# Kernel optimization log

Measured on AMD Instinct MI355X. Metric: run time of the kernel, lower is better.

Reference implementation:

```python
import jax, jax.numpy as jnp
import numpy as np

NUM_HEADS = 8  # from init_kwargs
SR = 2         # sr_ratio from init_kwargs


def layernorm(t, g, b, eps=1e-5):
    mu = jnp.mean(t, axis=-1, keepdims=True)
    var = jnp.mean((t - mu) ** 2, axis=-1, keepdims=True)
    return (t - mu) * jax.lax.rsqrt(var + eps) * g + b


def setup_inputs() -> dict:
    key = jax.random.key(0)
    ks = jax.random.split(key, 6)
    B, C = 4, 256
    Hx = Wx = 64
    Hz = Wz = 32
    N = Hz * Wz + Hx * Wx  # 5120 (template tokens first, then search tokens)
    s = 0.02
    return {
        "x": jax.random.normal(ks[0], (B, N, C), jnp.float32),
        "Wq": jax.random.normal(ks[1], (C, C), jnp.float32) * s,          # nn.Linear(dim, dim, bias=False)
        "Wkv": jax.random.normal(ks[2], (2 * C, C), jnp.float32) * s,     # nn.Linear(dim, 2*dim, bias=False)
        "Wsr": jax.random.normal(ks[3], (C, C, SR, SR), jnp.float32) * s, # Conv2d(dim, dim, k=sr, stride=sr) OIHW
        "bsr": jnp.zeros((C,), jnp.float32),
        "gamma": jnp.ones((C,), jnp.float32),
        "beta": jnp.zeros((C,), jnp.float32),
        "Wproj": jax.random.normal(ks[4], (C, C), jnp.float32) * s,
        "bproj": jnp.zeros((C,), jnp.float32),
        "H_x": Hx, "W_x": Wx, "H_z": Hz, "W_z": Wz,
    }


def reference(x, Wq, Wkv, Wsr, bsr, gamma, beta, Wproj, bproj, H_x, W_x, H_z, W_z):
    B, N, C = x.shape
    h = NUM_HEADS
    d = C // h
    scale = d ** -0.5
    Nz, Nx = H_z * W_z, H_x * W_x

    # q for all tokens: [B, h, N, d]
    q = (x @ Wq.T).reshape(B, N, h, d).transpose(0, 2, 1, 3)

    # spatial reduction (sr_ratio > 1 branch): strided conv + layernorm on each stream
    z_tok, x_tok = x[:, :Nz], x[:, Nz:]
    ker = jnp.transpose(Wsr, (2, 3, 1, 0))  # OIHW -> HWIO

    def sr_branch(t, H, W):
        img = t.reshape(B, H, W, C)  # NHWC; same layout as torch NCHW reshape
        out = jax.lax.conv_general_dilated(
            img, ker, window_strides=(SR, SR), padding="VALID",
            dimension_numbers=("NHWC", "HWIO", "NHWC")) + bsr
        out = out.reshape(B, -1, C)
        return layernorm(out, gamma, beta)

    x_ = sr_branch(x_tok, H_x, W_x)  # [B, (Hx/sr)*(Wx/sr), C]
    z_ = sr_branch(z_tok, H_z, W_z)  # [B, (Hz/sr)*(Wz/sr), C]
    zL = z_.shape[1]
    cat = jnp.concatenate([z_, x_], axis=1)  # [B, L, C]

    kv = (cat @ Wkv.T).reshape(B, -1, 2, h, d).transpose(2, 0, 3, 1, 4)  # [2, B, h, L, d]
    k, v = kv[0], kv[1]

    q_z, q_x = q[:, :, :Nz], q[:, :, Nz:]
    k_z, v_z = k[:, :, :zL], v[:, :, :zL]

    # template queries attend only to reduced template keys/values
    attn_z = jax.nn.softmax(jnp.einsum("bhqd,bhkd->bhqk", q_z, k_z) * scale, axis=-1)
    out_z = jnp.einsum("bhqk,bhkd->bhqd", attn_z, v_z).transpose(0, 2, 1, 3).reshape(B, Nz, C)

    # search queries attend to full (template+search) reduced keys/values
    attn_x = jax.nn.softmax(jnp.einsum("bhqd,bhkd->bhqk", q_x, k) * scale, axis=-1)
    out_x = jnp.einsum("bhqk,bhkd->bhqd", attn_x, v).transpose(0, 2, 1, 3).reshape(B, Nx, C)

    out = jnp.concatenate([out_z, out_x], axis=1)
    return out @ Wproj.T + bproj
```

## Files before the change

### kernel.cpp

```cpp
#include <hip/hip_runtime.h>
#include <hip/hip_bf16.h>
#include <cstddef>

#define BATCH 4
#define CCH 256
#define NHEAD 8
#define DHEAD 32
#define NZ 1024
#define NX 4096
#define NTOK 5120
#define LKV 1280
#define QC 0.25503486f

typedef __attribute__((ext_vector_type(8))) short bf16x8;
typedef __attribute__((ext_vector_type(4))) float floatx4;

__device__ inline short f2bf(float f) {
  __hip_bfloat16 h = __float2bfloat16(f);
  return __builtin_bit_cast(short, h);
}
__device__ inline unsigned int pk2(float a, float b) {
  unsigned int lo = (unsigned short)f2bf(a);
  unsigned int hi = (unsigned short)f2bf(b);
  return lo | (hi << 16);
}
__device__ inline unsigned int pk2f(float a, float b) {
  unsigned int ua = __builtin_bit_cast(unsigned int, a) + 0x8000u;
  unsigned int ub = __builtin_bit_cast(unsigned int, b) + 0x8000u;
  return __builtin_amdgcn_perm(ub, ua, 0x07060302u);
}
__device__ inline void cvt8(const float* __restrict__ src, short* __restrict__ dst, int i) {
  float4 v0 = ((const float4*)src)[i * 2];
  float4 v1 = ((const float4*)src)[i * 2 + 1];
  uint4 u;
  u.x = pk2(v0.x, v0.y); u.y = pk2(v0.z, v0.w);
  u.z = pk2(v1.x, v1.y); u.w = pk2(v1.z, v1.w);
  ((uint4*)dst)[i] = u;
}

__global__ __launch_bounds__(256) void prep_weights(const float* __restrict__ Wq,
                                                    const float* __restrict__ Wkv,
                                                    const float* __restrict__ Wproj,
                                                    const float* __restrict__ Wsr,
                                                    const float* __restrict__ x,
                                                    short* __restrict__ Wqb,
                                                    short* __restrict__ Wkvb,
                                                    short* __restrict__ Wprojb,
                                                    short* __restrict__ Wkb,
                                                    short* __restrict__ xb) {
  int blk = blockIdx.x, tid = threadIdx.x;
  if (blk < 32) {
    cvt8(Wq, Wqb, blk * 256 + tid);
  } else if (blk < 96) {
    cvt8(Wkv, Wkvb, (blk - 32) * 256 + tid);
  } else if (blk < 128) {
    cvt8(Wproj, Wprojb, (blk - 96) * 256 + tid);
  } else if (blk < 1152) {
    int i = (blk - 128) * 256 + tid;
    int co = i >> 10;
    int rem = i & 1023;
    int di = rem >> 9, dj = (rem >> 8) & 1, ci = rem & 255;
    Wkb[i] = f2bf(Wsr[((co * 256 + ci) * 2 + di) * 2 + dj]);
  } else {
    cvt8(x, xb, (blk - 1152) * 256 + tid);
  }
}

#define G64_DECL()                                                           \
  __shared__ short As[64][72];                                               \
  __shared__ short Bs[64][72];                                               \
  int tid = threadIdx.x;                                                     \
  int wave = tid >> 6, lg = (tid & 63) >> 4, lr = tid & 15;                  \
  int sr = tid >> 2, sc = tid & 3;                                           \
  floatx4 acc[4] = {{0.f,0.f,0.f,0.f},{0.f,0.f,0.f,0.f},                     \
                    {0.f,0.f,0.f,0.f},{0.f,0.f,0.f,0.f}};

#define G64_MFMA8()                                                          \
    __syncthreads();                                                         \
    {                                                                        \
      bf16x8 af0 = *(bf16x8*)&As[wave * 16 + lr][lg * 8];                    \
      bf16x8 af1 = *(bf16x8*)&As[wave * 16 + lr][32 + lg * 8];               \
      _Pragma("unroll") for (int n = 0; n < 4; ++n) {                        \
        bf16x8 bf0 = *(bf16x8*)&Bs[n * 16 + lr][lg * 8];                     \
        bf16x8 bf1 = *(bf16x8*)&Bs[n * 16 + lr][32 + lg * 8];                \
        acc[n] = __builtin_amdgcn_mfma_f32_16x16x32_bf16(af0, bf0, acc[n], 0, 0, 0); \
        acc[n] = __builtin_amdgcn_mfma_f32_16x16x32_bf16(af1, bf1, acc[n], 0, 0, 0); \
      }                                                                      \
    }

__global__ __launch_bounds__(256) void gemm_qconv(const short* __restrict__ xb,
                                                  const short* __restrict__ Wqb,
                                                  const short* __restrict__ Wkb,
                                                  short* __restrict__ qbf,
                                                  float* __restrict__ cat_pre) {
  G64_DECL()
  int bidx = blockIdx.x;
  if (bidx < 1280) {
    int bm = (bidx >> 2) * 64, bn = (bidx & 3) * 64;
    for (int k0 = 0; k0 < 256; k0 += 64) {
      bf16x8 a0 = *(const bf16x8*)&xb[(size_t)(bm + sr) * 256 + k0 + sc * 8];
      bf16x8 a1 = *(const bf16x8*)&xb[(size_t)(bm + sr) * 256 + k0 + (sc + 4) * 8];
      bf16x8 b0 = *(const bf16x8*)&Wqb[(size_t)(bn + sr) * 256 + k0 + sc * 8];
      bf16x8 b1 = *(const bf16x8*)&Wqb[(size_t)(bn + sr) * 256 + k0 + (sc + 4) * 8];
      __syncthreads();
      *(bf16x8*)&As[sr][sc * 8] = a0;
      *(bf16x8*)&As[sr][(sc + 4) * 8] = a1;
      *(bf16x8*)&Bs[sr][sc * 8] = b0;
      *(bf16x8*)&Bs[sr][(sc + 4) * 8] = b1;
      G64_MFMA8()
    }
#pragma unroll
    for (int n = 0; n < 4; ++n) {
      int c = bn + 16 * n + lr;
      int h = c >> 5, d = c & 31;
#pragma unroll
      for (int reg = 0; reg < 4; ++reg) {
        int m = bm + wave * 16 + 4 * lg + reg;
        int b = m / NTOK, tok = m - b * NTOK;
        qbf[((size_t)(b * 8 + h) * NTOK + tok) * 32 + d] = f2bf(acc[n][reg] * QC);
      }
    }
  } else {
    int idx = bidx - 1280;
    int mt = idx >> 2;
    int bm = mt * 64, bn = (idx & 3) * 64;
    int bq = mt / 20;
    int tloc = (mt % 20) * 64 + sr;
    for (int k0 = 0; k0 < 1024; k0 += 64) {
      int di = k0 >> 9, dj = (k0 >> 8) & 1;
      int srow;
      if (tloc < 256) {
        int oi = tloc >> 4, oj = tloc & 15;
        srow = bq * NTOK + (2 * oi + di) * 32 + (2 * oj + dj);
      } else {
        int tt = tloc - 256;
        int oi = tt >> 5, oj = tt & 31;
        srow = bq * NTOK + NZ + (2 * oi + di) * 64 + (2 * oj + dj);
      }
      int cb = k0 & 255;
      bf16x8 a0 = *(const bf16x8*)&xb[(size_t)srow * 256 + cb + sc * 8];
      bf16x8 a1 = *(const bf16x8*)&xb[(size_t)srow * 256 + cb + (sc + 4) * 8];
      bf16x8 b0 = *(const bf16x8*)&Wkb[(size_t)(bn + sr) * 1024 + k0 + sc * 8];
      bf16x8 b1 = *(const bf16x8*)&Wkb[(size_t)(bn + sr) * 1024 + k0 + (sc + 4) * 8];
      __syncthreads();
      *(bf16x8*)&As[sr][sc * 8] = a0;
      *(bf16x8*)&As[sr][(sc + 4) * 8] = a1;
      *(bf16x8*)&Bs[sr][sc * 8] = b0;
      *(bf16x8*)&Bs[sr][(sc + 4) * 8] = b1;
      G64_MFMA8()
    }
#pragma unroll
    for (int n = 0; n < 4; ++n) {
      int c = bn + 16 * n + lr;
#pragma unroll
      for (int reg = 0; reg < 4; ++reg) {
        int m = bm + wave * 16 + 4 * lg + reg;
        cat_pre[(size_t)m * 256 + c] = acc[n][reg];
      }
    }
  }
}

__global__ __launch_bounds__(256) void gemm_kv64(const short* __restrict__ A,
                                                 const short* __restrict__ Bm,
                                                 short* __restrict__ Kbf,
                                                 short* __restrict__ Vtb) {
  G64_DECL()
  int bm = blockIdx.y * 64, bn = blockIdx.x * 64;
  for (int k0 = 0; k0 < 256; k0 += 64) {
    bf16x8 a0 = *(const bf16x8*)&A[(size_t)(bm + sr) * 256 + k0 + sc * 8];
    bf16x8 a1 = *(const bf16x8*)&A[(size_t)(bm + sr) * 256 + k0 + (sc + 4) * 8];
    bf16x8 b0 = *(const bf16x8*)&Bm[(size_t)(bn + sr) * 256 + k0 + sc * 8];
    bf16x8 b1 = *(const bf16x8*)&Bm[(size_t)(bn + sr) * 256 + k0 + (sc + 4) * 8];
    __syncthreads();
    *(bf16x8*)&As[sr][sc * 8] = a0;
    *(bf16x8*)&As[sr][(sc + 4) * 8] = a1;
    *(bf16x8*)&Bs[sr][sc * 8] = b0;
    *(bf16x8*)&Bs[sr][(sc + 4) * 8] = b1;
    G64_MFMA8()
  }
#pragma unroll
  for (int n = 0; n < 4; ++n) {
    int c = bn + 16 * n + lr;
#pragma unroll
    for (int reg = 0; reg < 4; ++reg) {
      int m = bm + wave * 16 + 4 * lg + reg;
      int b = m / LKV, kvg = m - b * LKV;
      if (c < 256) {
        int h = c >> 5, d = c & 31;
        Kbf[((size_t)(b * 8 + h) * LKV + kvg) * 32 + d] = f2bf(acc[n][reg]);
      } else {
        int cc = c - 256;
        int h = cc >> 5, d = cc & 31;
        int tile = kvg >> 6, kvin = kvg & 63;
        Vtb[(((size_t)(b * 8 + h) * 20 + tile) * 32 + d) * 64 + kvin] = f2bf(acc[n][reg]);
      }
    }
  }
}

__global__ __launch_bounds__(256) void gemm_proj64(const short* __restrict__ A,
                                                   const short* __restrict__ Bm,
                                                   const float* __restrict__ bias,
                                                   float* __restrict__ Cm) {
  G64_DECL()
  int bm = blockIdx.y * 64, bn = blockIdx.x * 64;
  for (int k0 = 0; k0 < 256; k0 += 64) {
    bf16x8 a0 = *(const bf16x8*)&A[(size_t)(bm + sr) * 256 + k0 + sc * 8];
    bf16x8 a1 = *(const bf16x8*)&A[(size_t)(bm + sr) * 256 + k0 + (sc + 4) * 8];
    bf16x8 b0 = *(const bf16x8*)&Bm[(size_t)(bn + sr) * 256 + k0 + sc * 8];
    bf16x8 b1 = *(const bf16x8*)&Bm[(size_t)(bn + sr) * 256 + k0 + (sc + 4) * 8];
    __syncthreads();
    *(bf16x8*)&As[sr][sc * 8] = a0;
    *(bf16x8*)&As[sr][(sc + 4) * 8] = a1;
    *(bf16x8*)&Bs[sr][sc * 8] = b0;
    *(bf16x8*)&Bs[sr][(sc + 4) * 8] = b1;
    G64_MFMA8()
  }
#pragma unroll
  for (int n = 0; n < 4; ++n) {
    int c = bn + 16 * n + lr;
    float bv = bias[c];
#pragma unroll
    for (int reg = 0; reg < 4; ++reg) {
      int m = bm + wave * 16 + 4 * lg + reg;
      Cm[(size_t)m * 256 + c] = acc[n][reg] + bv;
    }
  }
}

__global__ __launch_bounds__(256) void ln_kernel(const float* __restrict__ cat_pre,
                                                 const float* __restrict__ bsr,
                                                 const float* __restrict__ gamma,
                                                 const float* __restrict__ beta,
                                                 short* __restrict__ catb) {
  int row = blockIdx.x * 4 + (threadIdx.x >> 6);
  int lane = threadIdx.x & 63;
  float4 v = *(const float4*)&cat_pre[(size_t)row * 256 + lane * 4];
  float4 bb = *(const float4*)&bsr[lane * 4];
  v.x += bb.x; v.y += bb.y; v.z += bb.z; v.w += bb.w;
  float s = (v.x + v.y) + (v.z + v.w);
#pragma unroll
  for (int mask = 1; mask < 64; mask <<= 1) s += __shfl_xor(s, mask, 64);
  float mu = s * (1.f / 256.f);
  float4 dv;
  dv.x = v.x - mu; dv.y = v.y - mu; dv.z = v.z - mu; dv.w = v.w - mu;
  float q = dv.x * dv.x + dv.y * dv.y + dv.z * dv.z + dv.w * dv.w;
#pragma unroll
  for (int mask = 1; mask < 64; mask <<= 1) q += __shfl_xor(q, mask, 64);
  float rs = rsqrtf(q * (1.f / 256.f) + 1e-5f);
  float4 g = *(const float4*)&gamma[lane * 4];
  float4 be = *(const float4*)&beta[lane * 4];
  uint2 st;
  st.x = pk2(dv.x * rs * g.x + be.x, dv.y * rs * g.y + be.y);
  st.y = pk2(dv.z * rs * g.z + be.z, dv.w * rs * g.w + be.w);
  *(uint2*)&catb[(size_t)row * 256 + lane * 4] = st;
}

__global__ __launch_bounds__(256) void attn_fused(const short* __restrict__ qbf,
                                                  const short* __restrict__ Kbf,
                                                  const short* __restrict__ Vtb,
                                                  short* __restrict__ attn_out) {
  int orig = blockIdx.x;
  int blk = (orig & 7) * 80 + (orig >> 3);
  int bh, q0, kvlen;
  if (blk < 512) {
    bh = blk >> 4; q0 = NZ + (blk & 15) * 256; kvlen = LKV;
  } else {
    int idx = blk - 512;
    bh = idx >> 2; q0 = (idx & 3) * 256; kvlen = 256;
  }
  int b = bh >> 3, hh = bh & 7;
  int tid = threadIdx.x;
  int wave = tid >> 6, lane = tid & 63, lg = lane >> 4, lr = lane & 15;

  __shared__ short Ps[4][64][72];

  int qtok = q0 + wave * 64;
  const short* qb = qbf + ((size_t)bh * NTOK + qtok) * 32;
  bf16x8 qf[4];
#pragma unroll
  for (int qi = 0; qi < 4; ++qi)
    qf[qi] = *(const bf16x8*)&qb[(16 * qi + lr) * 32 + lg * 8];

  const short* Kb = Kbf + (size_t)bh * LKV * 32;
  const short* Vb = Vtb + (size_t)bh * 20 * 2048;

  floatx4 oacc[4][2];
#pragma unroll
  for (int qi = 0; qi < 4; ++qi)
#pragma unroll
    for (int n = 0; n < 2; ++n) oacc[qi][n] = (floatx4){0.f, 0.f, 0.f, 0.f};
  float lsum[4] = {0.f, 0.f, 0.f, 0.f};

  bf16x8 kfc[4], vfc[2][2];
#pragma unroll
  for (int m = 0; m < 4; ++m)
    kfc[m] = *(const bf16x8*)&Kb[(size_t)(16 * m + lr) * 32 + lg * 8];
#pragma unroll
  for (int n = 0; n < 2; ++n)
#pragma unroll
    for (int kb = 0; kb < 2; ++kb)
      vfc[n][kb] = *(const bf16x8*)&Vb[(16 * n + lr) * 64 + kb * 32 + lg * 8];

  for (int l0 = 0; l0 < kvlen; l0 += 64) {
    __builtin_amdgcn_sched_barrier(0);
#pragma unroll
    for (int qi = 0; qi < 4; ++qi) {
      floatx4 st[4];
      __builtin_amdgcn_s_setprio(1);
#pragma unroll
      for (int m = 0; m < 4; ++m)
        st[m] = __builtin_amdgcn_mfma_f32_16x16x32_bf16(
            kfc[m], qf[qi], (floatx4){0.f, 0.f, 0.f, 0.f}, 0, 0, 0);
      __builtin_amdgcn_s_setprio(0);
      int pr = 16 * qi + lr;
#pragma unroll
      for (int m = 0; m < 4; ++m) {
        float p0 = __builtin_amdgcn_exp2f(st[m][0]);
        float p1 = __builtin_amdgcn_exp2f(st[m][1]);
        float p2 = __builtin_amdgcn_exp2f(st[m][2]);
        float p3 = __builtin_amdgcn_exp2f(st[m][3]);
        lsum[qi] += (p0 + p1) + (p2 + p3);
        uint2 w;
        w.x = pk2f(p0, p1);
        w.y = pk2f(p2, p3);
        *(uint2*)&Ps[wave][pr][16 * m + 4 * lg] = w;
      }
    }

    bf16x8 kfn[4], vfn[2][2];
    int l1 = l0 + 64;
    if (l1 < kvlen) {
      const short* Vbt = Vb + (l1 >> 6) * 2048;
#pragma unroll
      for (int m = 0; m < 4; ++m)
        kfn[m] = *(const bf16x8*)&Kb[(size_t)(l1 + 16 * m + lr) * 32 + lg * 8];
#pragma unroll
      for (int n = 0; n < 2; ++n)
#pragma unroll
        for (int kb = 0; kb < 2; ++kb)
          vfn[n][kb] = *(const bf16x8*)&Vbt[(16 * n + lr) * 64 + kb * 32 + lg * 8];
    }

    __builtin_amdgcn_sched_barrier(0);

    __builtin_amdgcn_s_setprio(1);
#pragma unroll
    for (int qi = 0; qi < 4; ++qi)
#pragma unroll
      for (int kb = 0; kb < 2; ++kb) {
        bf16x8 pf = *(bf16x8*)&Ps[wave][16 * qi + lr][kb * 32 + lg * 8];
#pragma unroll
        for (int n = 0; n < 2; ++n)
          oacc[qi][n] = __builtin_amdgcn_mfma_f32_16x16x32_bf16(pf, vfc[n][kb], oacc[qi][n], 0, 0, 0);
      }
    __builtin_amdgcn_s_setprio(0);

#pragma unroll
    for (int m = 0; m < 4; ++m) kfc[m] = kfn[m];
#pragma unroll
    for (int n = 0; n < 2; ++n)
#pragma unroll
      for (int kb = 0; kb < 2; ++kb) vfc[n][kb] = vfn[n][kb];
  }

#pragma unroll
  for (int qi = 0; qi < 4; ++qi) {
    lsum[qi] += __shfl_xor(lsum[qi], 16, 64);
    lsum[qi] += __shfl_xor(lsum[qi], 32, 64);
  }

#pragma unroll
  for (int qi = 0; qi < 4; ++qi)
#pragma unroll
    for (int reg = 0; reg < 4; ++reg) {
      float lv = __shfl(lsum[qi], 4 * lg + reg, 64);
      float inv = 1.f / lv;
      int gr = b * NTOK + qtok + 16 * qi + 4 * lg + reg;
      short* ob = attn_out + (size_t)gr * CCH + hh * DHEAD;
      ob[lr]      = f2bf(oacc[qi][0][reg] * inv);
      ob[16 + lr] = f2bf(oacc[qi][1][reg] * inv);
    }
}

extern "C" void kernel_launch(void* const* d_in, const int* in_sizes, int n_in,
                              void* d_out, int out_size, void* d_ws, size_t ws_size,
                              hipStream_t stream) {
  (void)in_sizes; (void)n_in; (void)out_size; (void)ws_size;
  const float* x     = (const float*)d_in[0];
  const float* Wq    = (const float*)d_in[1];
  const float* Wkv   = (const float*)d_in[2];
  const float* Wsr   = (const float*)d_in[3];
  const float* bsr   = (const float*)d_in[4];
  const float* gamma = (const float*)d_in[5];
  const float* beta  = (const float*)d_in[6];
  const float* Wproj = (const float*)d_in[7];
  const float* bproj = (const float*)d_in[8];
  float* out = (float*)d_out;
  float* ws  = (float*)d_ws;

  short* qbf      = (short*)ws;
  short* attn_out = (short*)(ws + 2621440);
  float* cat_pre  = ws + 7864320;
  short* catb     = (short*)(ws + 9175040);
  short* Kbf      = (short*)(ws + 9830400);
  short* Vtb      = (short*)(ws + 10485760);
  short* Wqb      = (short*)(ws + 11141120);
  short* Wkvb     = (short*)(ws + 11173888);
  short* Wkb      = (short*)(ws + 11239424);
  short* Wprojb   = (short*)(ws + 11370496);
  short* xb       = attn_out;

  prep_weights<<<3712, 256, 0, stream>>>(Wq, Wkv, Wproj, Wsr, x, Wqb, Wkvb, Wprojb, Wkb, xb);
  gemm_qconv<<<1600, 256, 0, stream>>>(xb, Wqb, Wkb, qbf, cat_pre);
  ln_kernel<<<1280, 256, 0, stream>>>(cat_pre, bsr, gamma, beta, catb);
  gemm_kv64<<<dim3(8, 80), 256, 0, stream>>>(catb, Wkvb, Kbf, Vtb);
  attn_fused<<<640, 256, 0, stream>>>(qbf, Kbf, Vtb, attn_out);
  gemm_proj64<<<dim3(4, 320), 256, 0, stream>>>(attn_out, Wprojb, bproj, out);
}
```

Baseline: 210.6 us.

## Fuse layernorm into KV GEMM and split attention into single-wave blocks

The separate layernorm kernel is removed. The KV GEMM now normalizes its 64 rows of cat_pre in registers and writes the full bf16 row block into LDS, then streams only the weight tiles. This drops one launch and the bf16 catb round trip to global memory, but each of the 8 column blocks now recomputes the same layernorm rows. The attention kernel goes from 4-wave blocks to 64-thread single-wave blocks (2560 blocks) with XCD-aware head mapping and no setprio, aiming for finer scheduling and occupancy.

```diff
diff --git a/kernel.cpp b/kernel.cpp
--- a/kernel.cpp
+++ b/kernel.cpp
@@ -161,23 +161,64 @@
   }
 }
 
-__global__ __launch_bounds__(256) void gemm_kv64(const short* __restrict__ A,
+__global__ __launch_bounds__(256) void gemm_kv64(const float* __restrict__ cat_pre,
+                                                 const float* __restrict__ bsr,
+                                                 const float* __restrict__ gamma,
+                                                 const float* __restrict__ beta,
                                                  const short* __restrict__ Bm,
                                                  short* __restrict__ Kbf,
                                                  short* __restrict__ Vtb) {
-  G64_DECL()
+  __shared__ short Af[64][264];
+  __shared__ short Bs[64][72];
+  int tid = threadIdx.x;
+  int wave = tid >> 6, lg = (tid & 63) >> 4, lr = tid & 15;
+  int sr = tid >> 2, sc = tid & 3;
+  int lane = tid & 63;
+  floatx4 acc[4] = {{0.f,0.f,0.f,0.f},{0.f,0.f,0.f,0.f},
+                    {0.f,0.f,0.f,0.f},{0.f,0.f,0.f,0.f}};
   int bm = blockIdx.y * 64, bn = blockIdx.x * 64;
+
+  float4 bb = *(const float4*)&bsr[lane * 4];
+  float4 g4 = *(const float4*)&gamma[lane * 4];
+  float4 be = *(const float4*)&beta[lane * 4];
+#pragma unroll
+  for (int i = 0; i < 16; ++i) {
+    int row = bm + wave * 16 + i;
+    float4 v = *(const float4*)&cat_pre[(size_t)row * 256 + lane * 4];
+    v.x += bb.x; v.y += bb.y; v.z += bb.z; v.w += bb.w;
+    float s = (v.x + v.y) + (v.z + v.w);
+#pragma unroll
+    for (int mask = 1; mask < 64; mask <<= 1) s += __shfl_xor(s, mask, 64);
+    float mu = s * (1.f / 256.f);
+    float4 dv;
+    dv.x = v.x - mu; dv.y = v.y - mu; dv.z = v.z - mu; dv.w = v.w - mu;
+    float q = dv.x * dv.x + dv.y * dv.y + dv.z * dv.z + dv.w * dv.w;
+#pragma unroll
+    for (int mask = 1; mask < 64; mask <<= 1) q += __shfl_xor(q, mask, 64);
+    float rs = rsqrtf(q * (1.f / 256.f) + 1e-5f);
+    uint2 st;
+    st.x = pk2(dv.x * rs * g4.x + be.x, dv.y * rs * g4.y + be.y);
+    st.y = pk2(dv.z * rs * g4.z + be.z, dv.w * rs * g4.w + be.w);
+    *(uint2*)&Af[wave * 16 + i][lane * 4] = st;
+  }
+  __syncthreads();
+
   for (int k0 = 0; k0 < 256; k0 += 64) {
-    bf16x8 a0 = *(const bf16x8*)&A[(size_t)(bm + sr) * 256 + k0 + sc * 8];
-    bf16x8 a1 = *(const bf16x8*)&A[(size_t)(bm + sr) * 256 + k0 + (sc + 4) * 8];
     bf16x8 b0 = *(const bf16x8*)&Bm[(size_t)(bn + sr) * 256 + k0 + sc * 8];
     bf16x8 b1 = *(const bf16x8*)&Bm[(size_t)(bn + sr) * 256 + k0 + (sc + 4) * 8];
     __syncthreads();
-    *(bf16x8*)&As[sr][sc * 8] = a0;
-    *(bf16x8*)&As[sr][(sc + 4) * 8] = a1;
     *(bf16x8*)&Bs[sr][sc * 8] = b0;
     *(bf16x8*)&Bs[sr][(sc + 4) * 8] = b1;
-    G64_MFMA8()
+    __syncthreads();
+    bf16x8 af0 = *(bf16x8*)&Af[wave * 16 + lr][k0 + lg * 8];
+    bf16x8 af1 = *(bf16x8*)&Af[wave * 16 + lr][k0 + 32 + lg * 8];
+#pragma unroll
+    for (int n = 0; n < 4; ++n) {
+      bf16x8 bf0 = *(bf16x8*)&Bs[n * 16 + lr][lg * 8];
+      bf16x8 bf1 = *(bf16x8*)&Bs[n * 16 + lr][32 + lg * 8];
+      acc[n] = __builtin_amdgcn_mfma_f32_16x16x32_bf16(af0, bf0, acc[n], 0, 0, 0);
+      acc[n] = __builtin_amdgcn_mfma_f32_16x16x32_bf16(af1, bf1, acc[n], 0, 0, 0);
+    }
   }
 #pragma unroll
   for (int n = 0; n < 4; ++n) {
@@ -229,54 +270,30 @@
   }
 }
 
-__global__ __launch_bounds__(256) void ln_kernel(const float* __restrict__ cat_pre,
-                                                 const float* __restrict__ bsr,
-                                                 const float* __restrict__ gamma,
-                                                 const float* __restrict__ beta,
-                                                 short* __restrict__ catb) {
-  int row = blockIdx.x * 4 + (threadIdx.x >> 6);
-  int lane = threadIdx.x & 63;
-  float4 v = *(const float4*)&cat_pre[(size_t)row * 256 + lane * 4];
-  float4 bb = *(const float4*)&bsr[lane * 4];
-  v.x += bb.x; v.y += bb.y; v.z += bb.z; v.w += bb.w;
-  float s = (v.x + v.y) + (v.z + v.w);
-#pragma unroll
-  for (int mask = 1; mask < 64; mask <<= 1) s += __shfl_xor(s, mask, 64);
-  float mu = s * (1.f / 256.f);
-  float4 dv;
-  dv.x = v.x - mu; dv.y = v.y - mu; dv.z = v.z - mu; dv.w = v.w - mu;
-  float q = dv.x * dv.x + dv.y * dv.y + dv.z * dv.z + dv.w * dv.w;
-#pragma unroll
-  for (int mask = 1; mask < 64; mask <<= 1) q += __shfl_xor(q, mask, 64);
-  float rs = rsqrtf(q * (1.f / 256.f) + 1e-5f);
-  float4 g = *(const float4*)&gamma[lane * 4];
-  float4 be = *(const float4*)&beta[lane * 4];
-  uint2 st;
-  st.x = pk2(dv.x * rs * g.x + be.x, dv.y * rs * g.y + be.y);
-  st.y = pk2(dv.z * rs * g.z + be.z, dv.w * rs * g.w + be.w);
-  *(uint2*)&catb[(size_t)row * 256 + lane * 4] = st;
-}
-
-__global__ __launch_bounds__(256) void attn_fused(const short* __restrict__ qbf,
-                                                  const short* __restrict__ Kbf,
-                                                  const short* __restrict__ Vtb,
-                                                  short* __restrict__ attn_out) {
+__global__ __launch_bounds__(64) void attn_fused(const short* __restrict__ qbf,
+                                                 const short* __restrict__ Kbf,
+                                                 const short* __restrict__ Vtb,
+                                                 short* __restrict__ attn_out) {
   int orig = blockIdx.x;
-  int blk = (orig & 7) * 80 + (orig >> 3);
+  int xcd = orig & 7, s = orig >> 3;
   int bh, q0, kvlen;
-  if (blk < 512) {
-    bh = blk >> 4; q0 = NZ + (blk & 15) * 256; kvlen = LKV;
+  if (s < 256) {
+    bh = xcd + 8 * (s >> 6);
+    q0 = NZ + (s & 63) * 64;
+    kvlen = LKV;
   } else {
-    int idx = blk - 512;
-    bh = idx >> 2; q0 = (idx & 3) * 256; kvlen = 256;
+    int s2 = s - 256;
+    bh = xcd + 8 * (s2 >> 4);
+    q0 = (s2 & 15) * 64;
+    kvlen = 256;
   }
   int b = bh >> 3, hh = bh & 7;
   int tid = threadIdx.x;
-  int wave = tid >> 6, lane = tid & 63, lg = lane >> 4, lr = lane & 15;
-
-  __shared__ short Ps[4][64][72];
-
-  int qtok = q0 + wave * 64;
+  int lane = tid & 63, lg = lane >> 4, lr = lane & 15;
+
+  __shared__ short Ps[64][72];
+
+  int qtok = q0;
   const short* qb = qbf + ((size_t)bh * NTOK + qtok) * 32;
   bf16x8 qf[4];
 #pragma unroll
@@ -308,12 +325,10 @@
 #pragma unroll
     for (int qi = 0; qi < 4; ++qi) {
       floatx4 st[4];
-      __builtin_amdgcn_s_setprio(1);
 #pragma unroll
       for (int m = 0; m < 4; ++m)
         st[m] = __builtin_amdgcn_mfma_f32_16x16x32_bf16(
             kfc[m], qf[qi], (floatx4){0.f, 0.f, 0.f, 0.f}, 0, 0, 0);
-      __builtin_amdgcn_s_setprio(0);
       int pr = 16 * qi + lr;
 #pragma unroll
       for (int m = 0; m < 4; ++m) {
@@ -325,7 +340,7 @@
         uint2 w;
         w.x = pk2f(p0, p1);
         w.y = pk2f(p2, p3);
-        *(uint2*)&Ps[wave][pr][16 * m + 4 * lg] = w;
+        *(uint2*)&Ps[pr][16 * m + 4 * lg] = w;
       }
     }
 
@@ -345,17 +360,15 @@
 
     __builtin_amdgcn_sched_barrier(0);
 
-    __builtin_amdgcn_s_setprio(1);
 #pragma unroll
     for (int qi = 0; qi < 4; ++qi)
 #pragma unroll
       for (int kb = 0; kb < 2; ++kb) {
-        bf16x8 pf = *(bf16x8*)&Ps[wave][16 * qi + lr][kb * 32 + lg * 8];
+        bf16x8 pf = *(bf16x8*)&Ps[16 * qi + lr][kb * 32 + lg * 8];
 #pragma unroll
         for (int n = 0; n < 2; ++n)
           oacc[qi][n] = __builtin_amdgcn_mfma_f32_16x16x32_bf16(pf, vfc[n][kb], oacc[qi][n], 0, 0, 0);
       }
-    __builtin_amdgcn_s_setprio(0);
 
 #pragma unroll
     for (int m = 0; m < 4; ++m) kfc[m] = kfn[m];
@@ -403,7 +416,6 @@
   short* qbf      = (short*)ws;
   short* attn_out = (short*)(ws + 2621440);
   float* cat_pre  = ws + 7864320;
-  short* catb     = (short*)(ws + 9175040);
   short* Kbf      = (short*)(ws + 9830400);
   short* Vtb      = (short*)(ws + 10485760);
   short* Wqb      = (short*)(ws + 11141120);
@@ -414,8 +426,7 @@
 
   prep_weights<<<3712, 256, 0, stream>>>(Wq, Wkv, Wproj, Wsr, x, Wqb, Wkvb, Wprojb, Wkb, xb);
   gemm_qconv<<<1600, 256, 0, stream>>>(xb, Wqb, Wkb, qbf, cat_pre);
-  ln_kernel<<<1280, 256, 0, stream>>>(cat_pre, bsr, gamma, beta, catb);
-  gemm_kv64<<<dim3(8, 80), 256, 0, stream>>>(catb, Wkvb, Kbf, Vtb);
-  attn_fused<<<640, 256, 0, stream>>>(qbf, Kbf, Vtb, attn_out);
+  gemm_kv64<<<dim3(8, 80), 256, 0, stream>>>(cat_pre, bsr, gamma, beta, Wkvb, Kbf, Vtb);
+  attn_fused<<<2560, 64, 0, stream>>>(qbf, Kbf, Vtb, attn_out);
   gemm_proj64<<<dim3(4, 320), 256, 0, stream>>>(attn_out, Wprojb, bproj, out);
 }
```

After: 190.8 us. 1.1x faster.

## Split attention into single-wave blocks and compute row sums via MFMA

Applied to the files above, without the earlier changes.

The attention kernel moves from 4-wave blocks over 256 queries to single-wave blocks over 64 queries, launched as 2560 blocks with an XCD-aware mapping that keeps each batch-head on one XCD. Softmax denominators now come from an extra MFMA against a ones vector instead of scalar adds plus shuffles. The probability packing uses the hardware v_cvt_pk_bf16_f32 instruction, and the setprio hints are removed. The aim is finer scheduling granularity, better L2 locality and fewer VALU ops, at the cost of extra MFMA work and more block launches.

```diff
diff --git a/kernel.cpp b/kernel.cpp
--- a/kernel.cpp
+++ b/kernel.cpp
@@ -24,10 +24,10 @@
   unsigned int hi = (unsigned short)f2bf(b);
   return lo | (hi << 16);
 }
-__device__ inline unsigned int pk2f(float a, float b) {
-  unsigned int ua = __builtin_bit_cast(unsigned int, a) + 0x8000u;
-  unsigned int ub = __builtin_bit_cast(unsigned int, b) + 0x8000u;
-  return __builtin_amdgcn_perm(ub, ua, 0x07060302u);
+__device__ inline unsigned int cvtpk(float a, float b) {
+  unsigned int r;
+  asm("v_cvt_pk_bf16_f32 %0, %1, %2" : "=v"(r) : "v"(a), "v"(b));
+  return r;
 }
 __device__ inline void cvt8(const float* __restrict__ src, short* __restrict__ dst, int i) {
   float4 v0 = ((const float4*)src)[i * 2];
@@ -257,26 +257,30 @@
   *(uint2*)&catb[(size_t)row * 256 + lane * 4] = st;
 }
 
-__global__ __launch_bounds__(256) void attn_fused(const short* __restrict__ qbf,
-                                                  const short* __restrict__ Kbf,
-                                                  const short* __restrict__ Vtb,
-                                                  short* __restrict__ attn_out) {
+__global__ __launch_bounds__(64) void attn_fused(const short* __restrict__ qbf,
+                                                 const short* __restrict__ Kbf,
+                                                 const short* __restrict__ Vtb,
+                                                 short* __restrict__ attn_out) {
   int orig = blockIdx.x;
-  int blk = (orig & 7) * 80 + (orig >> 3);
+  int xcd = orig & 7, s = orig >> 3;
   int bh, q0, kvlen;
-  if (blk < 512) {
-    bh = blk >> 4; q0 = NZ + (blk & 15) * 256; kvlen = LKV;
+  if (s < 256) {
+    bh = xcd + 8 * (s >> 6);
+    q0 = NZ + (s & 63) * 64;
+    kvlen = LKV;
   } else {
-    int idx = blk - 512;
-    bh = idx >> 2; q0 = (idx & 3) * 256; kvlen = 256;
+    int s2 = s - 256;
+    bh = xcd + 8 * (s2 >> 4);
+    q0 = (s2 & 15) * 64;
+    kvlen = 256;
   }
   int b = bh >> 3, hh = bh & 7;
   int tid = threadIdx.x;
-  int wave = tid >> 6, lane = tid & 63, lg = lane >> 4, lr = lane & 15;
-
-  __shared__ short Ps[4][64][72];
-
-  int qtok = q0 + wave * 64;
+  int lane = tid & 63, lg = lane >> 4, lr = lane & 15;
+
+  __shared__ short Ps[64][72];
+
+  int qtok = q0;
   const short* qb = qbf + ((size_t)bh * NTOK + qtok) * 32;
   bf16x8 qf[4];
 #pragma unroll
@@ -286,12 +290,17 @@
   const short* Kb = Kbf + (size_t)bh * LKV * 32;
   const short* Vb = Vtb + (size_t)bh * 20 * 2048;
 
+  const short onebf = (short)0x3F80;
+  bf16x8 onesb = {onebf, onebf, onebf, onebf, onebf, onebf, onebf, onebf};
+
   floatx4 oacc[4][2];
-#pragma unroll
-  for (int qi = 0; qi < 4; ++qi)
+  floatx4 lacc[4];
+#pragma unroll
+  for (int qi = 0; qi < 4; ++qi) {
+    lacc[qi] = (floatx4){0.f, 0.f, 0.f, 0.f};
 #pragma unroll
     for (int n = 0; n < 2; ++n) oacc[qi][n] = (floatx4){0.f, 0.f, 0.f, 0.f};
-  float lsum[4] = {0.f, 0.f, 0.f, 0.f};
+  }
 
   bf16x8 kfc[4], vfc[2][2];
 #pragma unroll
@@ -308,12 +317,10 @@
 #pragma unroll
     for (int qi = 0; qi < 4; ++qi) {
       floatx4 st[4];
-      __builtin_amdgcn_s_setprio(1);
 #pragma unroll
       for (int m = 0; m < 4; ++m)
         st[m] = __builtin_amdgcn_mfma_f32_16x16x32_bf16(
             kfc[m], qf[qi], (floatx4){0.f, 0.f, 0.f, 0.f}, 0, 0, 0);
-      __builtin_amdgcn_s_setprio(0);
       int pr = 16 * qi + lr;
 #pragma unroll
       for (int m = 0; m < 4; ++m) {
@@ -321,11 +328,10 @@
         float p1 = __builtin_amdgcn_exp2f(st[m][1]);
         float p2 = __builtin_amdgcn_exp2f(st[m][2]);
         float p3 = __builtin_amdgcn_exp2f(st[m][3]);
-        lsum[qi] += (p0 + p1) + (p2 + p3);
         uint2 w;
-        w.x = pk2f(p0, p1);
-        w.y = pk2f(p2, p3);
-        *(uint2*)&Ps[wave][pr][16 * m + 4 * lg] = w;
+        w.x = cvtpk(p0, p1);
+        w.y = cvtpk(p2, p3);
+        *(uint2*)&Ps[pr][16 * m + 4 * lg] = w;
       }
     }
 
@@ -345,17 +351,16 @@
 
     __builtin_amdgcn_sched_barrier(0);
 
-    __builtin_amdgcn_s_setprio(1);
 #pragma unroll
     for (int qi = 0; qi < 4; ++qi)
 #pragma unroll
       for (int kb = 0; kb < 2; ++kb) {
-        bf16x8 pf = *(bf16x8*)&Ps[wave][16 * qi + lr][kb * 32 + lg * 8];
+        bf16x8 pf = *(bf16x8*)&Ps[16 * qi + lr][kb * 32 + lg * 8];
 #pragma unroll
         for (int n = 0; n < 2; ++n)
           oacc[qi][n] = __builtin_amdgcn_mfma_f32_16x16x32_bf16(pf, vfc[n][kb], oacc[qi][n], 0, 0, 0);
-      }
-    __builtin_amdgcn_s_setprio(0);
+        lacc[qi] = __builtin_amdgcn_mfma_f32_16x16x32_bf16(pf, onesb, lacc[qi], 0, 0, 0);
+      }
 
 #pragma unroll
     for (int m = 0; m < 4; ++m) kfc[m] = kfn[m];
@@ -366,17 +371,10 @@
   }
 
 #pragma unroll
-  for (int qi = 0; qi < 4; ++qi) {
-    lsum[qi] += __shfl_xor(lsum[qi], 16, 64);
-    lsum[qi] += __shfl_xor(lsum[qi], 32, 64);
-  }
-
-#pragma unroll
   for (int qi = 0; qi < 4; ++qi)
 #pragma unroll
     for (int reg = 0; reg < 4; ++reg) {
-      float lv = __shfl(lsum[qi], 4 * lg + reg, 64);
-      float inv = 1.f / lv;
+      float inv = 1.f / lacc[qi][reg];
       int gr = b * NTOK + qtok + 16 * qi + 4 * lg + reg;
       short* ob = attn_out + (size_t)gr * CCH + hh * DHEAD;
       ob[lr]      = f2bf(oacc[qi][0][reg] * inv);
@@ -416,6 +414,6 @@
   gemm_qconv<<<1600, 256, 0, stream>>>(xb, Wqb, Wkb, qbf, cat_pre);
   ln_kernel<<<1280, 256, 0, stream>>>(cat_pre, bsr, gamma, beta, catb);
   gemm_kv64<<<dim3(8, 80), 256, 0, stream>>>(catb, Wkvb, Kbf, Vtb);
-  attn_fused<<<640, 256, 0, stream>>>(qbf, Kbf, Vtb, attn_out);
+  attn_fused<<<2560, 64, 0, stream>>>(qbf, Kbf, Vtb, attn_out);
   gemm_proj64<<<dim3(4, 320), 256, 0, stream>>>(attn_out, Wprojb, bproj, out);
 }
```

New measurement: 191.2 us. -9.2%, faster.

## Split attention KV range across two waves with LDS combine, smaller blocks

Applied to the files above, without the earlier changes.

The attention kernel now uses 128-thread blocks that each own 64 query rows. The KV sequence is split in half between the two waves, and the partial sums and row sums are combined through shared memory before one wave writes the output. The XCD-aware block mapping is reworked so each XCD handles the same heads, and the grid grows from 640 to 2560 blocks. This is meant to raise parallelism and balance the short template blocks against the long search blocks. In exchange it adds a combine step with a sync, doubles the Q loads per query row, and drops the setprio hints.

```diff
diff --git a/kernel.cpp b/kernel.cpp
--- a/kernel.cpp
+++ b/kernel.cpp
@@ -257,26 +257,33 @@
   *(uint2*)&catb[(size_t)row * 256 + lane * 4] = st;
 }
 
-__global__ __launch_bounds__(256) void attn_fused(const short* __restrict__ qbf,
+__global__ __launch_bounds__(128) void attn_fused(const short* __restrict__ qbf,
                                                   const short* __restrict__ Kbf,
                                                   const short* __restrict__ Vtb,
                                                   short* __restrict__ attn_out) {
   int orig = blockIdx.x;
-  int blk = (orig & 7) * 80 + (orig >> 3);
+  int xcd = orig & 7, s = orig >> 3;
   int bh, q0, kvlen;
-  if (blk < 512) {
-    bh = blk >> 4; q0 = NZ + (blk & 15) * 256; kvlen = LKV;
+  if (s < 256) {
+    bh = xcd + 8 * (s >> 6);
+    q0 = NZ + (s & 63) * 64;
+    kvlen = LKV;
   } else {
-    int idx = blk - 512;
-    bh = idx >> 2; q0 = (idx & 3) * 256; kvlen = 256;
+    int s2 = s - 256;
+    bh = xcd + 8 * (s2 >> 4);
+    q0 = (s2 & 15) * 64;
+    kvlen = 256;
   }
   int b = bh >> 3, hh = bh & 7;
   int tid = threadIdx.x;
   int wave = tid >> 6, lane = tid & 63, lg = lane >> 4, lr = lane & 15;
 
-  __shared__ short Ps[4][64][72];
-
-  int qtok = q0 + wave * 64;
+  __shared__ short Ps[2][64][72];
+
+  int half = kvlen >> 1;
+  int lbeg = wave * half, lend = lbeg + half;
+
+  int qtok = q0;
   const short* qb = qbf + ((size_t)bh * NTOK + qtok) * 32;
   bf16x8 qf[4];
 #pragma unroll
@@ -296,24 +303,25 @@
   bf16x8 kfc[4], vfc[2][2];
 #pragma unroll
   for (int m = 0; m < 4; ++m)
-    kfc[m] = *(const bf16x8*)&Kb[(size_t)(16 * m + lr) * 32 + lg * 8];
-#pragma unroll
-  for (int n = 0; n < 2; ++n)
-#pragma unroll
-    for (int kb = 0; kb < 2; ++kb)
-      vfc[n][kb] = *(const bf16x8*)&Vb[(16 * n + lr) * 64 + kb * 32 + lg * 8];
-
-  for (int l0 = 0; l0 < kvlen; l0 += 64) {
+    kfc[m] = *(const bf16x8*)&Kb[(size_t)(lbeg + 16 * m + lr) * 32 + lg * 8];
+  {
+    const short* Vb0 = Vb + (lbeg >> 6) * 2048;
+#pragma unroll
+    for (int n = 0; n < 2; ++n)
+#pragma unroll
+      for (int kb = 0; kb < 2; ++kb)
+        vfc[n][kb] = *(const bf16x8*)&Vb0[(16 * n + lr) * 64 + kb * 32 + lg * 8];
+  }
+
+  for (int l0 = lbeg; l0 < lend; l0 += 64) {
     __builtin_amdgcn_sched_barrier(0);
 #pragma unroll
     for (int qi = 0; qi < 4; ++qi) {
       floatx4 st[4];
-      __builtin_amdgcn_s_setprio(1);
 #pragma unroll
       for (int m = 0; m < 4; ++m)
         st[m] = __builtin_amdgcn_mfma_f32_16x16x32_bf16(
             kfc[m], qf[qi], (floatx4){0.f, 0.f, 0.f, 0.f}, 0, 0, 0);
-      __builtin_amdgcn_s_setprio(0);
       int pr = 16 * qi + lr;
 #pragma unroll
       for (int m = 0; m < 4; ++m) {
@@ -331,7 +339,7 @@
 
     bf16x8 kfn[4], vfn[2][2];
     int l1 = l0 + 64;
-    if (l1 < kvlen) {
+    if (l1 < lend) {
       const short* Vbt = Vb + (l1 >> 6) * 2048;
 #pragma unroll
       for (int m = 0; m < 4; ++m)
@@ -345,7 +353,6 @@
 
     __builtin_amdgcn_sched_barrier(0);
 
-    __builtin_amdgcn_s_setprio(1);
 #pragma unroll
     for (int qi = 0; qi < 4; ++qi)
 #pragma unroll
@@ -355,7 +362,6 @@
         for (int n = 0; n < 2; ++n)
           oacc[qi][n] = __builtin_amdgcn_mfma_f32_16x16x32_bf16(pf, vfc[n][kb], oacc[qi][n], 0, 0, 0);
       }
-    __builtin_amdgcn_s_setprio(0);
 
 #pragma unroll
     for (int m = 0; m < 4; ++m) kfc[m] = kfn[m];
@@ -365,23 +371,50 @@
       for (int kb = 0; kb < 2; ++kb) vfc[n][kb] = vfn[n][kb];
   }
 
-#pragma unroll
-  for (int qi = 0; qi < 4; ++qi) {
-    lsum[qi] += __shfl_xor(lsum[qi], 16, 64);
-    lsum[qi] += __shfl_xor(lsum[qi], 32, 64);
-  }
-
-#pragma unroll
-  for (int qi = 0; qi < 4; ++qi)
-#pragma unroll
-    for (int reg = 0; reg < 4; ++reg) {
-      float lv = __shfl(lsum[qi], 4 * lg + reg, 64);
-      float inv = 1.f / lv;
-      int gr = b * NTOK + qtok + 16 * qi + 4 * lg + reg;
-      short* ob = attn_out + (size_t)gr * CCH + hh * DHEAD;
-      ob[lr]      = f2bf(oacc[qi][0][reg] * inv);
-      ob[16 + lr] = f2bf(oacc[qi][1][reg] * inv);
-    }
+  float* comb = (float*)&Ps[1][0][0];
+  if (wave == 1) {
+    float* p = comb + lane * 36;
+#pragma unroll
+    for (int qi = 0; qi < 4; ++qi) {
+      p[qi * 9] = lsum[qi];
+#pragma unroll
+      for (int n = 0; n < 2; ++n)
+#pragma unroll
+        for (int reg = 0; reg < 4; ++reg)
+          p[qi * 9 + 1 + n * 4 + reg] = oacc[qi][n][reg];
+    }
+  }
+  __syncthreads();
+  if (wave == 0) {
+    const float* p = comb + lane * 36;
+#pragma unroll
+    for (int qi = 0; qi < 4; ++qi) {
+      lsum[qi] += p[qi * 9];
+#pragma unroll
+      for (int n = 0; n < 2; ++n)
+#pragma unroll
+        for (int reg = 0; reg < 4; ++reg)
+          oacc[qi][n][reg] += p[qi * 9 + 1 + n * 4 + reg];
+    }
+
+#pragma unroll
+    for (int qi = 0; qi < 4; ++qi) {
+      lsum[qi] += __shfl_xor(lsum[qi], 16, 64);
+      lsum[qi] += __shfl_xor(lsum[qi], 32, 64);
+    }
+
+#pragma unroll
+    for (int qi = 0; qi < 4; ++qi)
+#pragma unroll
+      for (int reg = 0; reg < 4; ++reg) {
+        float lv = __shfl(lsum[qi], 4 * lg + reg, 64);
+        float inv = 1.f / lv;
+        int gr = b * NTOK + qtok + 16 * qi + 4 * lg + reg;
+        short* ob = attn_out + (size_t)gr * CCH + hh * DHEAD;
+        ob[lr]      = f2bf(oacc[qi][0][reg] * inv);
+        ob[16 + lr] = f2bf(oacc[qi][1][reg] * inv);
+      }
+  }
 }
 
 extern "C" void kernel_launch(void* const* d_in, const int* in_sizes, int n_in,
@@ -416,6 +449,6 @@
   gemm_qconv<<<1600, 256, 0, stream>>>(xb, Wqb, Wkb, qbf, cat_pre);
   ln_kernel<<<1280, 256, 0, stream>>>(cat_pre, bsr, gamma, beta, catb);
   gemm_kv64<<<dim3(8, 80), 256, 0, stream>>>(catb, Wkvb, Kbf, Vtb);
-  attn_fused<<<640, 256, 0, stream>>>(qbf, Kbf, Vtb, attn_out);
+  attn_fused<<<2560, 128, 0, stream>>>(qbf, Kbf, Vtb, attn_out);
   gemm_proj64<<<dim3(4, 320), 256, 0, stream>>>(attn_out, Wprojb, bproj, out);
 }
```

Result: faster. 190.1 us (-9.7%).
